# Kernel tuning notes

Measured on AMD Instinct MI355X. Metric: run time of the kernel, lower is better.

Reference implementation:

```python
import jax, jax.numpy as jnp
import numpy as np

N = 8388608  # batch size

def _xor(a, b):
    return a + b - 2.0 * a * b

def _or(a, b):
    return a + b - a * b

def setup_inputs() -> dict:
    key = jax.random.key(0)
    k1, k2 = jax.random.split(key)
    # binary 0/1 inputs as float32 (SNN spike values)
    A = jnp.round(jax.random.uniform(k1, (N, 8), dtype=jnp.float32))
    B = jnp.round(jax.random.uniform(k2, (N, 8), dtype=jnp.float32))
    Bin = jnp.zeros((N, 1), dtype=jnp.float32)
    return {"A": A, "B": B, "Bin": Bin}

def reference(A, B, Bin):
    """8-bit ripple-borrow subtractor A - B. Index 7 is the LSB.
    XOR(a,b)=a+b-2ab, AND=ab, OR=a+b-ab, NOT=1-a on 0/1 values."""
    borrow = Bin  # [N, 1]
    diffs = [None] * 8
    for i in range(7, -1, -1):  # LSB (7) -> MSB (0)
        a_i = A[..., i:i + 1]
        b_i = B[..., i:i + 1]
        diff = _xor(_xor(a_i, b_i), borrow)
        not_a = 1.0 - a_i
        borrow = _or(_or(not_a * b_i, not_a * borrow), b_i * borrow)
        diffs[i] = diff
    return jnp.concatenate(diffs, axis=-1), borrow
```

## Files before the change

### kernel.cpp

```cpp
#include <hip/hip_runtime.h>

__global__ __launch_bounds__(256) void sub8_kernel(
    const float4* __restrict__ A4, const float4* __restrict__ B4,
    const float* __restrict__ Bin, float4* __restrict__ D4,
    float* __restrict__ Bout, int n)
{
    int stride = gridDim.x * blockDim.x;
    for (int i = blockIdx.x * blockDim.x + threadIdx.x; i < n; i += stride) {
        float4 a0 = A4[2 * i];
        float4 a1 = A4[2 * i + 1];
        float4 b0 = B4[2 * i];
        float4 b1 = B4[2 * i + 1];
        bool borrow = Bin[i] != 0.0f;

        float av[8] = {a0.x, a0.y, a0.z, a0.w, a1.x, a1.y, a1.z, a1.w};
        float bv[8] = {b0.x, b0.y, b0.z, b0.w, b1.x, b1.y, b1.z, b1.w};
        float dv[8];

        #pragma unroll
        for (int j = 7; j >= 0; --j) {
            bool ai = av[j] != 0.0f;
            bool bi = bv[j] != 0.0f;
            bool diff = (ai ^ bi) ^ borrow;
            bool na = !ai;
            borrow = (na && bi) || (na && borrow) || (bi && borrow);
            dv[j] = diff ? 1.0f : 0.0f;
        }

        D4[2 * i]     = make_float4(dv[0], dv[1], dv[2], dv[3]);
        D4[2 * i + 1] = make_float4(dv[4], dv[5], dv[6], dv[7]);
        Bout[i] = borrow ? 1.0f : 0.0f;
    }
}

extern "C" void kernel_launch(void* const* d_in, const int* in_sizes, int n_in,
                              void* d_out, int out_size, void* d_ws, size_t ws_size,
                              hipStream_t stream) {
    const float* A   = (const float*)d_in[0];
    const float* B   = (const float*)d_in[1];
    const float* Bin = (const float*)d_in[2];
    int n = in_sizes[0] / 8;

    float* D    = (float*)d_out;
    float* Bout = D + (size_t)n * 8;

    const int block = 256;
    int grid = (n + block - 1) / block;
    if (grid > 2048) grid = 2048;

    sub8_kernel<<<grid, block, 0, stream>>>(
        (const float4*)A, (const float4*)B, Bin, (float4*)D, Bout, n);
}
```

Before: 170.4 us.

## Split each row across two lanes with carry-select borrow and shuffle

Each 8-bit row is now handled by two adjacent threads, each loading one float4 of A and B. Each thread computes its 4-bit half for both possible borrow-ins, and the low half's borrow-out is passed to the high-half thread via __shfl_xor. This gives contiguous per-lane float4 accesses, meant to improve coalescing and memory-level parallelism in a bandwidth-bound kernel, at the cost of redundant ALU work and one cross-lane shuffle. It relies on paired threads sharing a wavefront and staying in step in the grid-stride loop, which holds because the stride is even.

```diff
diff --git a/kernel.cpp b/kernel.cpp
--- a/kernel.cpp
+++ b/kernel.cpp
@@ -1,35 +1,59 @@
 #include <hip/hip_runtime.h>
 
+
+typedef float f32x4 __attribute__((ext_vector_type(4)));
+
+__device__ __forceinline__ void half_ripple(const f32x4 a, const f32x4 b, bool bin,
+                                            f32x4& d, bool& bout)
+{
+    float av[4] = {a.x, a.y, a.z, a.w};
+    float bv[4] = {b.x, b.y, b.z, b.w};
+    float dv[4];
+    bool borrow = bin;
+    #pragma unroll
+    for (int j = 3; j >= 0; --j) {
+        bool ai = av[j] != 0.0f;
+        bool bi = bv[j] != 0.0f;
+        bool diff = (ai ^ bi) ^ borrow;
+        bool na = !ai;
+        borrow = (na && bi) || (na && borrow) || (bi && borrow);
+        dv[j] = diff ? 1.0f : 0.0f;
+    }
+    d = (f32x4){dv[0], dv[1], dv[2], dv[3]};
+    bout = borrow;
+}
+
 __global__ __launch_bounds__(256) void sub8_kernel(
-    const float4* __restrict__ A4, const float4* __restrict__ B4,
-    const float* __restrict__ Bin, float4* __restrict__ D4,
-    float* __restrict__ Bout, int n)
+    const f32x4* __restrict__ A4, const f32x4* __restrict__ B4,
+    const float* __restrict__ Bin, f32x4* __restrict__ D4,
+    float* __restrict__ Bout, int n2 )
 {
-    int stride = gridDim.x * blockDim.x;
-    for (int i = blockIdx.x * blockDim.x + threadIdx.x; i < n; i += stride) {
-        float4 a0 = A4[2 * i];
-        float4 a1 = A4[2 * i + 1];
-        float4 b0 = B4[2 * i];
-        float4 b1 = B4[2 * i + 1];
-        bool borrow = Bin[i] != 0.0f;
+    const int stride = gridDim.x * blockDim.x;
+    for (int t = blockIdx.x * blockDim.x + threadIdx.x; t < n2; t += stride) {
+        const int  r   = t >> 1;
+        const bool odd = (t & 1) != 0;
 
-        float av[8] = {a0.x, a0.y, a0.z, a0.w, a1.x, a1.y, a1.z, a1.w};
-        float bv[8] = {b0.x, b0.y, b0.z, b0.w, b1.x, b1.y, b1.z, b1.w};
-        float dv[8];
+        f32x4 a = A4[t];
+        f32x4 b = B4[t];
+        float binf = Bin[r];
 
-        #pragma unroll
-        for (int j = 7; j >= 0; --j) {
-            bool ai = av[j] != 0.0f;
-            bool bi = bv[j] != 0.0f;
-            bool diff = (ai ^ bi) ^ borrow;
-            bool na = !ai;
-            borrow = (na && bi) || (na && borrow) || (bi && borrow);
-            dv[j] = diff ? 1.0f : 0.0f;
+        f32x4 d0, d1;
+        bool bo0, bo1;
+        half_ripple(a, b, false, d0, bo0);
+        half_ripple(a, b, true,  d1, bo1);
+
+        bool bin_low   = binf != 0.0f;
+        bool bout_low  = bin_low ? bo1 : bo0;
+        unsigned x     = __shfl_xor((unsigned)bout_low, 1);
+        bool myborrow  = odd ? bin_low : (x != 0);
+
+        f32x4 d = myborrow ? d1 : d0;
+        D4[t] = d;
+
+        if (!odd) {
+            bool bfin = myborrow ? bo1 : bo0;
+            Bout[r] = bfin ? 1.0f : 0.0f;
         }
-
-        D4[2 * i]     = make_float4(dv[0], dv[1], dv[2], dv[3]);
-        D4[2 * i + 1] = make_float4(dv[4], dv[5], dv[6], dv[7]);
-        Bout[i] = borrow ? 1.0f : 0.0f;
     }
 }
 
@@ -39,15 +63,16 @@
     const float* A   = (const float*)d_in[0];
     const float* B   = (const float*)d_in[1];
     const float* Bin = (const float*)d_in[2];
-    int n = in_sizes[0] / 8;
+    int n  = in_sizes[0] / 8;
+    int n2 = n * 2;
 
     float* D    = (float*)d_out;
     float* Bout = D + (size_t)n * 8;
 
     const int block = 256;
-    int grid = (n + block - 1) / block;
+    int grid = (n2 + block - 1) / block;
     if (grid > 2048) grid = 2048;
 
     sub8_kernel<<<grid, block, 0, stream>>>(
-        (const float4*)A, (const float4*)B, Bin, (float4*)D, Bout, n);
+        (const f32x4*)A, (const f32x4*)B, Bin, (f32x4*)D, Bout, n2);
 }
```

Measured after the change: 177.9 us. +4.4%, slower.

## Split each row across two lanes with carry-select borrow and shuffle

Applied to the files above, without the earlier changes.

Each row's eight bits are now processed by two adjacent threads, each handling four bits and computing both borrow-in cases. The low half's borrow-out is passed with a lane shuffle to pick the high half's result. The logic uses bitwise operations on the raw float bit patterns, and the grid-stride loop is replaced by one thread per half row. This aims for fully contiguous 16-byte per-lane accesses and more memory parallelism, but relies on inputs being exactly 0.0 or 1.0 bit patterns.

```diff
diff --git a/kernel.cpp b/kernel.cpp
--- a/kernel.cpp
+++ b/kernel.cpp
@@ -1,53 +1,67 @@
 #include <hip/hip_runtime.h>
 
+
+typedef unsigned int u32;
+typedef u32 u32x4 __attribute__((ext_vector_type(4)));
+#define FONE 0x3F800000u
+
 __global__ __launch_bounds__(256) void sub8_kernel(
-    const float4* __restrict__ A4, const float4* __restrict__ B4,
-    const float* __restrict__ Bin, float4* __restrict__ D4,
-    float* __restrict__ Bout, int n)
+    const u32x4* __restrict__ A4, const u32x4* __restrict__ B4,
+    const u32* __restrict__ Bin, u32x4* __restrict__ D4,
+    u32* __restrict__ Bout, int n2 )
 {
-    int stride = gridDim.x * blockDim.x;
-    for (int i = blockIdx.x * blockDim.x + threadIdx.x; i < n; i += stride) {
-        float4 a0 = A4[2 * i];
-        float4 a1 = A4[2 * i + 1];
-        float4 b0 = B4[2 * i];
-        float4 b1 = B4[2 * i + 1];
-        bool borrow = Bin[i] != 0.0f;
+    int t = blockIdx.x * blockDim.x + threadIdx.x;
+    if (t >= n2) return;
+    const bool odd = (t & 1) != 0;
+    const int  r   = t >> 1;
 
-        float av[8] = {a0.x, a0.y, a0.z, a0.w, a1.x, a1.y, a1.z, a1.w};
-        float bv[8] = {b0.x, b0.y, b0.z, b0.w, b1.x, b1.y, b1.z, b1.w};
-        float dv[8];
+    u32x4 a = A4[t];
+    u32x4 b = B4[t];
+    u32 binw = Bin[r];
 
-        #pragma unroll
-        for (int j = 7; j >= 0; --j) {
-            bool ai = av[j] != 0.0f;
-            bool bi = bv[j] != 0.0f;
-            bool diff = (ai ^ bi) ^ borrow;
-            bool na = !ai;
-            borrow = (na && bi) || (na && borrow) || (bi && borrow);
-            dv[j] = diff ? 1.0f : 0.0f;
-        }
+    u32 av[4] = {a.x, a.y, a.z, a.w};
+    u32 bv[4] = {b.x, b.y, b.z, b.w};
+    u32 d0v[4], d1v[4];
+    u32 bor0 = 0u, bor1 = FONE;
+    #pragma unroll
+    for (int j = 3; j >= 0; --j) {
+        u32 na = av[j] ^ FONE;
+        u32 x  = av[j] ^ bv[j];
+        u32 g  = na & bv[j];
+        u32 p  = na | bv[j];
+        d0v[j] = x ^ bor0;
+        d1v[j] = x ^ bor1;
+        bor0 = g | (p & bor0);
+        bor1 = g | (p & bor1);
+    }
 
-        D4[2 * i]     = make_float4(dv[0], dv[1], dv[2], dv[3]);
-        D4[2 * i + 1] = make_float4(dv[4], dv[5], dv[6], dv[7]);
-        Bout[i] = borrow ? 1.0f : 0.0f;
-    }
+    u32 bout_low = binw ? bor1 : bor0;
+    u32 xs = __shfl_xor(bout_low, 1);
+    u32 myborrow = odd ? binw : xs;
+
+    u32x4 d = myborrow ? (u32x4){d1v[0], d1v[1], d1v[2], d1v[3]}
+                       : (u32x4){d0v[0], d0v[1], d0v[2], d0v[3]};
+    D4[t] = d;
+
+    if (!odd)
+        Bout[r] = myborrow ? bor1 : bor0;
 }
 
 extern "C" void kernel_launch(void* const* d_in, const int* in_sizes, int n_in,
                               void* d_out, int out_size, void* d_ws, size_t ws_size,
                               hipStream_t stream) {
-    const float* A   = (const float*)d_in[0];
-    const float* B   = (const float*)d_in[1];
-    const float* Bin = (const float*)d_in[2];
-    int n = in_sizes[0] / 8;
+    const u32* A   = (const u32*)d_in[0];
+    const u32* B   = (const u32*)d_in[1];
+    const u32* Bin = (const u32*)d_in[2];
+    int n  = in_sizes[0] / 8;
+    int n2 = n * 2;
 
-    float* D    = (float*)d_out;
-    float* Bout = D + (size_t)n * 8;
+    u32* D    = (u32*)d_out;
+    u32* Bout = D + (size_t)n * 8;
 
     const int block = 256;
-    int grid = (n + block - 1) / block;
-    if (grid > 2048) grid = 2048;
+    int grid = (n2 + block - 1) / block;
 
     sub8_kernel<<<grid, block, 0, stream>>>(
-        (const float4*)A, (const float4*)B, Bin, (float4*)D, Bout, n);
+        (const u32x4*)A, (const u32x4*)B, Bin, (u32x4*)D, Bout, n2);
 }
```

Measured after the change: 154.3 us. -9.4%, faster.
